# Performance work log

Hardware: AMD Instinct MI355X
Metric: run time of the kernel (lower is better)

The kernel has to match this reference:

```python
import jax, jax.numpy as jnp
import numpy as np

BN_EPS = 1e-5

def setup_inputs() -> dict:
    key = jax.random.key(0)
    k1, k2 = jax.random.split(key)
    B, C, H, W, K = 256, 2048, 7, 7, 16
    featmap = jax.random.normal(k1, (B, C, H, W), dtype=jnp.float32)
    w16 = jax.random.normal(k2, (K, C), dtype=jnp.float32) * 0.02  # 1x1 conv weight
    bn_gamma = jnp.ones((K,), jnp.float32)
    bn_beta = jnp.zeros((K,), jnp.float32)
    bn_mean = jnp.zeros((K,), jnp.float32)
    bn_var = jnp.ones((K,), jnp.float32)
    return {"featmap": featmap, "w16": w16, "bn_gamma": bn_gamma,
            "bn_beta": bn_beta, "bn_mean": bn_mean, "bn_var": bn_var}

def reference(featmap, w16, bn_gamma, bn_beta, bn_mean, bn_var):
    # featmap: [B, 2048, 7, 7]; 1x1 conv -> featcov16: [B, 16, 7, 7]
    featcov16 = jnp.einsum('bchw,kc->bkhw', featmap, w16)
    # BatchNorm2d(16), inference-style with running stats
    inv = bn_gamma / jnp.sqrt(bn_var + BN_EPS)
    featcov16 = featcov16 * inv[None, :, None, None] + (bn_beta - bn_mean * inv)[None, :, None, None]
    # Loop-free bilinear pooling: original repeats featcov16[:,i] to 2048 ch,
    # multiplies with featmap, and AvgPool2d(7) -> mean over HxW.
    HW = featmap.shape[2] * featmap.shape[3]
    feat_matrix = jnp.einsum('bkhw,bchw->bkc', featcov16, featmap) / HW  # [B,16,2048]
    bp_out_feat = feat_matrix.reshape(feat_matrix.shape[0], -1)  # [B, 32768]
    return bp_out_feat
```

## Files before the change

kernel.cpp:

```cpp
#include <hip/hip_runtime.h>

#define BATCH 256
#define CDIM  2048
#define HW    49
#define KDIM  16
#define CHUNK 512
#define TILE  128
#define ROWP  52
#define WROWP 132

__global__ __launch_bounds__(256) void pconv_kernel(
    const float* __restrict__ fm, const float* __restrict__ w16,
    float* __restrict__ Ppart)
{
    __shared__ float fm_t[TILE * ROWP + 16];
    __shared__ float w_t[KDIM * WROWP];

    const int tid = threadIdx.x;
    const int b   = blockIdx.x >> 2;
    const int q   = blockIdx.x & 3;
    const int c0  = q * CHUNK;
    const int h4  = tid & 15;
    const int k   = tid >> 4;

    float acc0 = 0.f, acc1 = 0.f, acc2 = 0.f, acc3 = 0.f;

    const float* fmb = fm + (size_t)b * CDIM * HW;

    for (int tile = 0; tile < CHUNK / TILE; ++tile) {
        const int ct = c0 + tile * TILE;
        __syncthreads();
        const float4* src = (const float4*)(fmb + ct * HW);
        for (int i = tid; i < (TILE * HW) / 4; i += 256) {
            float4 v = src[i];
            int e = i * 4;
            int cl = e / HW; int h = e - cl * HW; fm_t[cl * ROWP + h] = v.x;
            e++; cl = e / HW; h = e - cl * HW;    fm_t[cl * ROWP + h] = v.y;
            e++; cl = e / HW; h = e - cl * HW;    fm_t[cl * ROWP + h] = v.z;
            e++; cl = e / HW; h = e - cl * HW;    fm_t[cl * ROWP + h] = v.w;
        }
        for (int i = tid; i < KDIM * TILE; i += 256) {
            int kk = i >> 7; int cc = i & 127;
            w_t[kk * WROWP + cc] = w16[kk * CDIM + ct + cc];
        }
        __syncthreads();
        #pragma unroll 4
        for (int cc = 0; cc < TILE; cc += 4) {
            float4 wv = *(const float4*)&w_t[k * WROWP + cc];
            float4 f0 = *(const float4*)&fm_t[(cc + 0) * ROWP + 4 * h4];
            float4 f1 = *(const float4*)&fm_t[(cc + 1) * ROWP + 4 * h4];
            float4 f2 = *(const float4*)&fm_t[(cc + 2) * ROWP + 4 * h4];
            float4 f3 = *(const float4*)&fm_t[(cc + 3) * ROWP + 4 * h4];
            acc0 += f0.x * wv.x + f1.x * wv.y + f2.x * wv.z + f3.x * wv.w;
            acc1 += f0.y * wv.x + f1.y * wv.y + f2.y * wv.z + f3.y * wv.w;
            acc2 += f0.z * wv.x + f1.z * wv.y + f2.z * wv.z + f3.z * wv.w;
            acc3 += f0.w * wv.x + f1.w * wv.y + f2.w * wv.z + f3.w * wv.w;
        }
    }

    float* dst = Ppart + (size_t)blockIdx.x * 784 + k * HW;
    const int hwb = 4 * h4;
    if (hwb + 0 < HW) dst[hwb + 0] = acc0;
    if (hwb + 1 < HW) dst[hwb + 1] = acc1;
    if (hwb + 2 < HW) dst[hwb + 2] = acc2;
    if (hwb + 3 < HW) dst[hwb + 3] = acc3;
}

__global__ __launch_bounds__(256) void bp_kernel(
    const float* __restrict__ fm, const float* __restrict__ Ppart,
    const float* __restrict__ gamma, const float* __restrict__ beta,
    const float* __restrict__ mean, const float* __restrict__ var,
    float* __restrict__ out)
{
    __shared__ float Pt[HW * KDIM];

    const int tid = threadIdx.x;
    const int b   = blockIdx.x >> 3;
    const int c0  = (blockIdx.x & 7) * 256;

    for (int p = tid; p < 784; p += 256) {
        const float* pp = Ppart + (size_t)(b * 4) * 784 + p;
        float s = pp[0] + pp[784] + pp[2 * 784] + pp[3 * 784];
        int kk = p / HW; int hw = p - kk * HW;
        float inv   = gamma[kk] * rsqrtf(var[kk] + 1e-5f);
        float shift = beta[kk] - mean[kk] * inv;
        Pt[hw * KDIM + kk] = (s * inv + shift) * (1.0f / 49.0f);
    }
    __syncthreads();

    const int c = c0 + tid;
    const float* row = fm + ((size_t)b * CDIM + c) * HW;

    float acc[16];
    #pragma unroll
    for (int i = 0; i < 16; ++i) acc[i] = 0.f;

    #pragma unroll 7
    for (int hw = 0; hw < HW; ++hw) {
        float f = row[hw];
        const float4* pv = (const float4*)&Pt[hw * KDIM];
        float4 p0 = pv[0], p1 = pv[1], p2 = pv[2], p3 = pv[3];
        acc[0]  += p0.x * f; acc[1]  += p0.y * f; acc[2]  += p0.z * f; acc[3]  += p0.w * f;
        acc[4]  += p1.x * f; acc[5]  += p1.y * f; acc[6]  += p1.z * f; acc[7]  += p1.w * f;
        acc[8]  += p2.x * f; acc[9]  += p2.y * f; acc[10] += p2.z * f; acc[11] += p2.w * f;
        acc[12] += p3.x * f; acc[13] += p3.y * f; acc[14] += p3.z * f; acc[15] += p3.w * f;
    }

    float* ob = out + (size_t)b * (KDIM * CDIM) + c;
    #pragma unroll
    for (int kk = 0; kk < 16; ++kk) ob[kk * CDIM] = acc[kk];
}

extern "C" void kernel_launch(void* const* d_in, const int* in_sizes, int n_in,
                              void* d_out, int out_size, void* d_ws, size_t ws_size,
                              hipStream_t stream) {
    const float* fm    = (const float*)d_in[0];
    const float* w16   = (const float*)d_in[1];
    const float* gamma = (const float*)d_in[2];
    const float* beta  = (const float*)d_in[3];
    const float* mean  = (const float*)d_in[4];
    const float* var   = (const float*)d_in[5];
    float* out   = (float*)d_out;
    float* Ppart = (float*)d_ws;

    pconv_kernel<<<BATCH * 4, 256, 0, stream>>>(fm, w16, Ppart);
    bp_kernel<<<BATCH * 8, 256, 0, stream>>>(fm, Ppart, gamma, beta, mean, var, out);
}
```

Baseline: 229.8 us.

## Register-block pconv over all K with LDS reduction; stage bp featmap rows in LDS

In pconv, each thread now keeps accumulators for all 16 output channels over a slice of 8 input channels, and w is transposed so each thread reads it as four float4 loads. The 16 channel-slice partials are then summed through shared memory. This cuts LDS reads per FMA but adds a reduction phase and raises register pressure. In bp, each block copies its 256x49 featmap slab into shared memory with coalesced float4 loads, replacing strided per-thread row reads, at the cost of about 50KB of LDS per block and lower occupancy.

After: 215.2 us. -6.3%, faster.

```diff
diff --git a/kernel.cpp b/kernel.cpp
--- a/kernel.cpp
+++ b/kernel.cpp
@@ -7,23 +7,26 @@
 #define CHUNK 512
 #define TILE  128
 #define ROWP  52
-#define WROWP 132
 
 __global__ __launch_bounds__(256) void pconv_kernel(
     const float* __restrict__ fm, const float* __restrict__ w16,
     float* __restrict__ Ppart)
 {
-    __shared__ float fm_t[TILE * ROWP + 16];
-    __shared__ float w_t[KDIM * WROWP];
+    __shared__ __align__(16) float fm_t[TILE * ROWP + 16];
+    __shared__ __align__(16) float w_t[TILE * KDIM];
 
     const int tid = threadIdx.x;
     const int b   = blockIdx.x >> 2;
     const int q   = blockIdx.x & 3;
     const int c0  = q * CHUNK;
     const int h4  = tid & 15;
-    const int k   = tid >> 4;
+    const int cs  = tid >> 4;
 
-    float acc0 = 0.f, acc1 = 0.f, acc2 = 0.f, acc3 = 0.f;
+    float acc[KDIM][4];
+    #pragma unroll
+    for (int k = 0; k < KDIM; ++k) {
+        acc[k][0] = 0.f; acc[k][1] = 0.f; acc[k][2] = 0.f; acc[k][3] = 0.f;
+    }
 
     const float* fmb = fm + (size_t)b * CDIM * HW;
 
@@ -41,29 +44,49 @@
         }
         for (int i = tid; i < KDIM * TILE; i += 256) {
             int kk = i >> 7; int cc = i & 127;
-            w_t[kk * WROWP + cc] = w16[kk * CDIM + ct + cc];
+            w_t[cc * KDIM + kk] = w16[kk * CDIM + ct + cc];
         }
         __syncthreads();
-        #pragma unroll 4
-        for (int cc = 0; cc < TILE; cc += 4) {
-            float4 wv = *(const float4*)&w_t[k * WROWP + cc];
-            float4 f0 = *(const float4*)&fm_t[(cc + 0) * ROWP + 4 * h4];
-            float4 f1 = *(const float4*)&fm_t[(cc + 1) * ROWP + 4 * h4];
-            float4 f2 = *(const float4*)&fm_t[(cc + 2) * ROWP + 4 * h4];
-            float4 f3 = *(const float4*)&fm_t[(cc + 3) * ROWP + 4 * h4];
-            acc0 += f0.x * wv.x + f1.x * wv.y + f2.x * wv.z + f3.x * wv.w;
-            acc1 += f0.y * wv.x + f1.y * wv.y + f2.y * wv.z + f3.y * wv.w;
-            acc2 += f0.z * wv.x + f1.z * wv.y + f2.z * wv.z + f3.z * wv.w;
-            acc3 += f0.w * wv.x + f1.w * wv.y + f2.w * wv.z + f3.w * wv.w;
+        #pragma unroll 2
+        for (int j = 0; j < 8; ++j) {
+            const int cc = cs * 8 + j;
+            float4 f = *(const float4*)&fm_t[cc * ROWP + 4 * h4];
+            const float4* wq = (const float4*)&w_t[cc * KDIM];
+            float wv[16];
+            *(float4*)&wv[0]  = wq[0];
+            *(float4*)&wv[4]  = wq[1];
+            *(float4*)&wv[8]  = wq[2];
+            *(float4*)&wv[12] = wq[3];
+            #pragma unroll
+            for (int k = 0; k < 16; ++k) {
+                acc[k][0] += wv[k] * f.x;
+                acc[k][1] += wv[k] * f.y;
+                acc[k][2] += wv[k] * f.z;
+                acc[k][3] += wv[k] * f.w;
+            }
         }
     }
 
-    float* dst = Ppart + (size_t)blockIdx.x * 784 + k * HW;
-    const int hwb = 4 * h4;
-    if (hwb + 0 < HW) dst[hwb + 0] = acc0;
-    if (hwb + 1 < HW) dst[hwb + 1] = acc1;
-    if (hwb + 2 < HW) dst[hwb + 2] = acc2;
-    if (hwb + 3 < HW) dst[hwb + 3] = acc3;
+    __syncthreads();
+    float* red = fm_t;
+    for (int r = 0; r < 4; ++r) {
+        #pragma unroll
+        for (int kk = 0; kk < 4; ++kk)
+            #pragma unroll
+            for (int hl = 0; hl < 4; ++hl)
+                red[cs * 272 + h4 * 17 + kk * 4 + hl] = acc[r * 4 + kk][hl];
+        __syncthreads();
+        const int kp = r * 4 + (tid >> 6);
+        const int hw = tid & 63;
+        if (hw < HW) {
+            float s = 0.f;
+            const int base = (hw >> 2) * 17 + (tid >> 6) * 4 + (hw & 3);
+            #pragma unroll
+            for (int c = 0; c < 16; ++c) s += red[c * 272 + base];
+            Ppart[(size_t)blockIdx.x * 784 + kp * HW + hw] = s;
+        }
+        __syncthreads();
+    }
 }
 
 __global__ __launch_bounds__(256) void bp_kernel(
@@ -72,7 +95,8 @@
     const float* __restrict__ mean, const float* __restrict__ var,
     float* __restrict__ out)
 {
-    __shared__ float Pt[HW * KDIM];
+    __shared__ __align__(16) float Pt[HW * KDIM];
+    __shared__ __align__(16) float fm_s[256 * HW];
 
     const int tid = threadIdx.x;
     const int b   = blockIdx.x >> 3;
@@ -80,21 +104,26 @@
 
     for (int p = tid; p < 784; p += 256) {
         const float* pp = Ppart + (size_t)(b * 4) * 784 + p;
-        float s = pp[0] + pp[784] + pp[2 * 784] + pp[3 * 784];
+        float s = pp[0] + pp[784] + pp[1568] + pp[2352];
         int kk = p / HW; int hw = p - kk * HW;
         float inv   = gamma[kk] * rsqrtf(var[kk] + 1e-5f);
         float shift = beta[kk] - mean[kk] * inv;
         Pt[hw * KDIM + kk] = (s * inv + shift) * (1.0f / 49.0f);
     }
+
+    {
+        const float4* src = (const float4*)(fm + ((size_t)b * CDIM + c0) * HW);
+        float4* dst = (float4*)fm_s;
+        #pragma unroll 7
+        for (int i = tid; i < (256 * HW) / 4; i += 256) dst[i] = src[i];
+    }
     __syncthreads();
-
-    const int c = c0 + tid;
-    const float* row = fm + ((size_t)b * CDIM + c) * HW;
 
     float acc[16];
     #pragma unroll
     for (int i = 0; i < 16; ++i) acc[i] = 0.f;
 
+    const float* row = fm_s + tid * HW;
     #pragma unroll 7
     for (int hw = 0; hw < HW; ++hw) {
         float f = row[hw];
@@ -106,7 +135,7 @@
         acc[12] += p3.x * f; acc[13] += p3.y * f; acc[14] += p3.z * f; acc[15] += p3.w * f;
     }
 
-    float* ob = out + (size_t)b * (KDIM * CDIM) + c;
+    float* ob = out + (size_t)b * (KDIM * CDIM) + c0 + tid;
     #pragma unroll
     for (int kk = 0; kk < 16; ++kk) ob[kk * CDIM] = acc[kk];
 }
```
